# Kernel optimization log

Measured on AMD Instinct MI355X. Metric: run time of the kernel, lower is better.

The kernel has to match this reference:

```python
import jax, jax.numpy as jnp
import numpy as np

B, P, D, C = 1024, 4, 512, 128  # batch, parts, feat_dim, num_classes


def setup_inputs() -> dict:
    key = jax.random.key(0)
    k1, k2 = jax.random.split(key)
    # scale 0.05 keeps dot products O(1) so exp() stays in fp32 range
    inputs = jax.random.normal(k1, (B, P, D), dtype=jnp.float32) * 0.05
    targets = jax.random.randint(k2, (B,), 0, C, dtype=jnp.int64)
    return {"inputs": inputs, "targets": targets}


def _npairs_loss(inputs, targets):
    b, p, d = inputs.shape
    n = b * p
    X = inputs.reshape(n, d)
    t = jnp.repeat(targets, p)              # (n,) class label per row
    parts = jnp.tile(jnp.arange(p), b)      # (n,) part id per row
    prod = X @ X.T                          # (n, n) similarities

    sc = t[:, None] == t[None, :]           # same class
    sp = parts[:, None] == parts[None, :]   # same attention part
    s_sadc = (~sc) & sp
    s_dasc = sc & (~sp)
    s_dadc = (~sc) & (~sp)

    e_pos = jnp.exp(prod)                   # exp(neg) terms
    e_neg = jnp.exp(-prod)                  # exp(-pos) terms

    def group_loss(pos_mask, neg_mask):
        # sum_i sum_{j in pos_i} log(1 + sum_{k in neg_i} exp(prod[i,k] - prod[i,j]))
        # = sum log1p(S_i * exp(-prod[i,j])) with S_i = sum_{k in neg_i} exp(prod[i,k])
        S = jnp.sum(jnp.where(neg_mask, e_pos, 0.0), axis=1)        # (n,)
        terms = jnp.where(pos_mask, jnp.log1p(S[:, None] * e_neg), 0.0)
        return jnp.sum(terms)

    loss_sadc = group_loss(s_sadc, s_dadc)
    loss_dasc = group_loss(s_dasc, s_dadc)
    # NOTE: original returns loss_sadc twice and never uses loss_sasc (bug kept for fidelity)
    return (loss_sadc + loss_sadc + loss_dasc) / n


def reference(inputs, targets):
    return _npairs_loss(inputs, targets)
```

## Files before the change

### kernel.cpp

```cpp
#include <hip/hip_runtime.h>
#include <stdint.h>

#define GLOBAL_AS __attribute__((address_space(1)))
#define LDS_AS    __attribute__((address_space(3)))

typedef __attribute__((ext_vector_type(8))) __bf16 bf16x8;
typedef __attribute__((ext_vector_type(4))) float  f32x4;

static_assert(sizeof(bf16x8) == 16, "bf16x8 must be 16B");

constexpr int N  = 4096;
constexpr int DK = 512;


__global__ void k_convert(const float* __restrict__ X, __bf16* __restrict__ Xb,
                          const int* __restrict__ tbuf, int* __restrict__ cls) {
    if (blockIdx.x == 1024) {
        __shared__ int is64;
        const int t = threadIdx.x;
        if (t == 0) is64 = 1;
        __syncthreads();
        if (tbuf[4 * t + 1] != 0 || tbuf[4 * t + 3] != 0) is64 = 0;
        __syncthreads();
        const int f = is64;
#pragma unroll
        for (int q = 0; q < 4; ++q) {
            const int ti = 4 * t + q;
            const int v = tbuf[f ? 2 * ti : ti];
            cls[4 * ti + 0] = v; cls[4 * ti + 1] = v;
            cls[4 * ti + 2] = v; cls[4 * ti + 3] = v;
        }
        return;
    }
    int idx = blockIdx.x * blockDim.x + threadIdx.x;
    const float4* s = (const float4*)X;
    float4 a = s[2 * idx + 0];
    float4 b = s[2 * idx + 1];
    bf16x8 o;
    o[0] = (__bf16)a.x; o[1] = (__bf16)a.y; o[2] = (__bf16)a.z; o[3] = (__bf16)a.w;
    o[4] = (__bf16)b.x; o[5] = (__bf16)b.y; o[6] = (__bf16)b.z; o[7] = (__bf16)b.w;
    *(bf16x8*)(Xb + 8 * idx) = o;
}

__launch_bounds__(512, 4)
__global__ void k_main(const __bf16* __restrict__ Xb, const int* __restrict__ cls,
                       float* __restrict__ partials) {
    __shared__ __align__(16) __bf16 As[2][128 * 64];
    __shared__ __align__(16) __bf16 Bs[2][128 * 64];
    __shared__ float4 accR[4][128];
    __shared__ float4 accC[2][128];
    __shared__ int rowcls[128], colcls[128];

    const int tid  = threadIdx.x;
    const int lane = tid & 63;
    const int wid  = tid >> 6;
    const int wr   = wid >> 2;
    const int wc   = wid & 3;

    const int bid = blockIdx.x;
    int rt = (int)((sqrtf(8.0f * (float)bid + 1.0f) - 1.0f) * 0.5f);
    while (((rt + 1) * (rt + 2)) / 2 <= bid) ++rt;
    while ((rt * (rt + 1)) / 2 > bid) --rt;
    const int g  = bid - (rt * (rt + 1)) / 2;
    const int i0 = rt * 128;
    const int j0 = g * 128;
    const bool offdiag = (rt != g);

    if (tid < 128) {
        rowcls[tid] = cls[i0 + tid];
        colcls[tid] = cls[j0 + tid];
    }

    f32x4 acc[4][2] = {};

    const char* xb   = (const char*)Xb;
    const int   srow = tid >> 3;
    const int   skb  = ((tid & 7) ^ (srow & 7)) * 16;
    const int   ldst = wid * 1024;
    const int   rA   = lane & 15;
    const int   kgrp = lane >> 4;

#define STAGE(buf, kt)                                                                         \
    {                                                                                          \
        const size_t kb0 = (size_t)(kt) * 128;                                                 \
        char* AsB = (char*)(&As[(buf)][0]);                                                    \
        char* BsB = (char*)(&Bs[(buf)][0]);                                                    \
        _Pragma("unroll")                                                                      \
        for (int t = 0; t < 2; ++t) {                                                          \
            __builtin_amdgcn_global_load_lds(                                                  \
                (const GLOBAL_AS void*)(xb + (size_t)(i0 + t * 64 + srow) * 1024 + kb0 + skb), \
                (LDS_AS void*)(AsB + t * 8192 + ldst), 16, 0, 0);                              \
            __builtin_amdgcn_global_load_lds(                                                  \
                (const GLOBAL_AS void*)(xb + (size_t)(j0 + t * 64 + srow) * 1024 + kb0 + skb), \
                (LDS_AS void*)(BsB + t * 8192 + ldst), 16, 0, 0);                              \
        }                                                                                      \
    }

    STAGE(0, 0);
    __syncthreads();

    int cur = 0;
#pragma unroll
    for (int kt = 0; kt < DK / 64; ++kt) {
        if (kt < DK / 64 - 1) STAGE(cur ^ 1, kt + 1);
        const char* A_ = (const char*)(&As[cur][0]);
        const char* B_ = (const char*)(&Bs[cur][0]);
#pragma unroll
        for (int kk = 0; kk < 2; ++kk) {
            bf16x8 af[4];
            bf16x8 bg[2];
#pragma unroll
            for (int m = 0; m < 4; ++m) {
                const int r = wr * 64 + m * 16 + rA;
                af[m] = *(const bf16x8*)(A_ + r * 128 + (((kk * 4 + kgrp) ^ (r & 7)) * 16));
            }
#pragma unroll
            for (int n = 0; n < 2; ++n) {
                const int r = wc * 32 + n * 16 + rA;
                bg[n] = *(const bf16x8*)(B_ + r * 128 + (((kk * 4 + kgrp) ^ (r & 7)) * 16));
            }
#pragma unroll
            for (int m = 0; m < 4; ++m)
#pragma unroll
                for (int n = 0; n < 2; ++n)
                    acc[m][n] = __builtin_amdgcn_mfma_f32_16x16x32_bf16(af[m], bg[n],
                                                                        acc[m][n], 0, 0, 0);
        }
        if (kt < DK / 64 - 1) {
            __syncthreads();
            cur ^= 1;
        }
    }
#undef STAGE

    const int pj = rA & 3;
    int cj[2];
#pragma unroll
    for (int n = 0; n < 2; ++n) cj[n] = colcls[wc * 32 + n * 16 + rA];
    float cS[2] = {0.f, 0.f}, cP[2] = {0.f, 0.f}, cE[2] = {0.f, 0.f}, cW[2] = {0.f, 0.f};

#pragma unroll
    for (int m = 0; m < 4; ++m) {
        const int rbase = wr * 64 + m * 16 + kgrp * 4;
        int ci[4];
#pragma unroll
        for (int r = 0; r < 4; ++r) ci[r] = rowcls[rbase + r];
        float sS[4] = {0.f, 0.f, 0.f, 0.f};
        float sP[4] = {0.f, 0.f, 0.f, 0.f};
        float sE[4] = {0.f, 0.f, 0.f, 0.f};
        float sW[4] = {0.f, 0.f, 0.f, 0.f};
#pragma unroll
        for (int n = 0; n < 2; ++n) {
#pragma unroll
            for (int r = 0; r < 4; ++r) {
                const float p  = acc[m][n][r];
                const float ep = __expf(p);
                const bool sc = (ci[r] == cj[n]);
                const bool sp = (r == pj);
                if (!sc && !sp) { sS[r] += ep; cS[n] += ep; }
                const float w = (!sc && sp) ? 2.f : ((sc && !sp) ? 1.f : 0.f);
                sP[r] += w * p;  sE[r] += w * ep;  sW[r] += w;
                cP[n] += w * p;  cE[n] += w * ep;  cW[n] += w;
            }
        }
#pragma unroll
        for (int r = 0; r < 4; ++r) {
            float vS = sS[r], vP = sP[r], vE = sE[r], vW = sW[r];
#pragma unroll
            for (int off = 1; off < 16; off <<= 1) {
                vS += __shfl_xor(vS, off);
                vP += __shfl_xor(vP, off);
                vE += __shfl_xor(vE, off);
                vW += __shfl_xor(vW, off);
            }
            if (rA == 0) accR[wc][rbase + r] = make_float4(vS, vP, vE, vW);
        }
    }

    {
#pragma unroll
        for (int n = 0; n < 2; ++n) {
            float vS = cS[n], vP = cP[n], vE = cE[n], vW = cW[n];
            vS += __shfl_xor(vS, 16); vS += __shfl_xor(vS, 32);
            vP += __shfl_xor(vP, 16); vP += __shfl_xor(vP, 32);
            vE += __shfl_xor(vE, 16); vE += __shfl_xor(vE, 32);
            vW += __shfl_xor(vW, 16); vW += __shfl_xor(vW, 32);
            if (kgrp == 0) accC[wr][wc * 32 + n * 16 + rA] = make_float4(vS, vP, vE, vW);
        }
    }

    __syncthreads();
    if (tid < 128) {
        float4 a0 = accR[0][tid], a1 = accR[1][tid], a2 = accR[2][tid], a3 = accR[3][tid];
        float4 o = make_float4(a0.x + a1.x + a2.x + a3.x, a0.y + a1.y + a2.y + a3.y,
                               a0.z + a1.z + a2.z + a3.z, a0.w + a1.w + a2.w + a3.w);
        ((float4*)partials)[(size_t)(i0 + tid) * 32 + g] = o;
        if (offdiag) {
            float4 c0 = accC[0][tid], c1 = accC[1][tid];
            float4 oc = make_float4(c0.x + c1.x, c0.y + c1.y, c0.z + c1.z, c0.w + c1.w);
            ((float4*)partials)[(size_t)(j0 + tid) * 32 + rt] = oc;
        }
    }
}

__global__ void k_rowloss(const float* __restrict__ partials, float* __restrict__ blockSums) {
    __shared__ float red[16];
    const int tid = threadIdx.x;
    const int sub = tid & 15;
    const int row = blockIdx.x * 16 + (tid >> 4);

    const float4* p = ((const float4*)partials) + (size_t)row * 32;
    float4 a = p[sub];
    float4 b = p[sub + 16];
    float S = a.x + b.x, P = a.y + b.y, E = a.z + b.z, W = a.w + b.w;
#pragma unroll
    for (int off = 1; off < 16; off <<= 1) {
        S += __shfl_xor(S, off);
        P += __shfl_xor(P, off);
        E += __shfl_xor(E, off);
        W += __shfl_xor(W, off);
    }
    if (sub == 0) red[tid >> 4] = W * logf(S) - P + E / S;
    __syncthreads();
    if (tid == 0) {
        float s = 0.f;
#pragma unroll
        for (int r = 0; r < 16; ++r) s += red[r];
        blockSums[blockIdx.x] = s;
    }
}

__global__ void k_final2(const float* __restrict__ blockSums, float* __restrict__ out) {
    const int t = threadIdx.x;
    float v = blockSums[t] + blockSums[t + 64] + blockSums[t + 128] + blockSums[t + 192];
#pragma unroll
    for (int off = 1; off < 64; off <<= 1) v += __shfl_xor(v, off);
    if (t == 0) out[0] = v / (float)N;
}

extern "C" void kernel_launch(void* const* d_in, const int* in_sizes, int n_in,
                              void* d_out, int out_size, void* d_ws, size_t ws_size,
                              hipStream_t stream) {
    const float* X = (const float*)d_in[0];
    const int*   T = (const int*)d_in[1];
    float* out = (float*)d_out;

    char* ws = (char*)d_ws;
    __bf16* Xb     = (__bf16*)ws;
    int*    cls    = (int*)(ws + (size_t)4 * 1024 * 1024);
    float*  parts  = (float*)(ws + (size_t)4 * 1024 * 1024 + 16 * 1024);
    float*  bsums  = (float*)ws;

    hipLaunchKernelGGL(k_convert, dim3(1025), dim3(256), 0, stream, X, Xb, T, cls);
    hipLaunchKernelGGL(k_main,    dim3(528),  dim3(512), 0, stream, Xb, cls, parts);
    hipLaunchKernelGGL(k_rowloss, dim3(256),  dim3(256), 0, stream, parts, bsums);
    hipLaunchKernelGGL(k_final2,  dim3(1),    dim3(64),  0, stream, bsums, out);
}
```

Before: 59.12 us.

## Transpose MFMA output layout and remap block ids across XCDs

```diff
diff --git a/kernel.cpp b/kernel.cpp
--- a/kernel.cpp
+++ b/kernel.cpp
@@ -57,7 +57,7 @@
     const int wr   = wid >> 2;
     const int wc   = wid & 3;
 
-    const int bid = blockIdx.x;
+    const int bid = (blockIdx.x & 7) * 66 + (blockIdx.x >> 3);
     int rt = (int)((sqrtf(8.0f * (float)bid + 1.0f) - 1.0f) * 0.5f);
     while (((rt + 1) * (rt + 2)) / 2 <= bid) ++rt;
     while ((rt * (rt + 1)) / 2 > bid) --rt;
@@ -123,7 +123,7 @@
             for (int m = 0; m < 4; ++m)
 #pragma unroll
                 for (int n = 0; n < 2; ++n)
-                    acc[m][n] = __builtin_amdgcn_mfma_f32_16x16x32_bf16(af[m], bg[n],
+                    acc[m][n] = __builtin_amdgcn_mfma_f32_16x16x32_bf16(bg[n], af[m],
                                                                         acc[m][n], 0, 0, 0);
         }
         if (kt < DK / 64 - 1) {
@@ -133,60 +133,54 @@
     }
 #undef STAGE
 
-    const int pj = rA & 3;
-    int cj[2];
-#pragma unroll
-    for (int n = 0; n < 2; ++n) cj[n] = colcls[wc * 32 + n * 16 + rA];
-    float cS[2] = {0.f, 0.f}, cP[2] = {0.f, 0.f}, cE[2] = {0.f, 0.f}, cW[2] = {0.f, 0.f};
-
-#pragma unroll
-    for (int m = 0; m < 4; ++m) {
-        const int rbase = wr * 64 + m * 16 + kgrp * 4;
-        int ci[4];
-#pragma unroll
-        for (int r = 0; r < 4; ++r) ci[r] = rowcls[rbase + r];
-        float sS[4] = {0.f, 0.f, 0.f, 0.f};
-        float sP[4] = {0.f, 0.f, 0.f, 0.f};
-        float sE[4] = {0.f, 0.f, 0.f, 0.f};
-        float sW[4] = {0.f, 0.f, 0.f, 0.f};
-#pragma unroll
-        for (int n = 0; n < 2; ++n) {
-#pragma unroll
-            for (int r = 0; r < 4; ++r) {
+    const int pi = rA & 3;
+    int ci[4];
+#pragma unroll
+    for (int m = 0; m < 4; ++m) ci[m] = rowcls[wr * 64 + m * 16 + rA];
+
+    float rS[4] = {0.f, 0.f, 0.f, 0.f};
+    float rP[4] = {0.f, 0.f, 0.f, 0.f};
+    float rE[4] = {0.f, 0.f, 0.f, 0.f};
+    float rW[4] = {0.f, 0.f, 0.f, 0.f};
+
+#pragma unroll
+    for (int n = 0; n < 2; ++n) {
+#pragma unroll
+        for (int r = 0; r < 4; ++r) {
+            const int cj = colcls[wc * 32 + n * 16 + kgrp * 4 + r];
+            float cS = 0.f, cP = 0.f, cE = 0.f, cW = 0.f;
+#pragma unroll
+            for (int m = 0; m < 4; ++m) {
                 const float p  = acc[m][n][r];
                 const float ep = __expf(p);
-                const bool sc = (ci[r] == cj[n]);
-                const bool sp = (r == pj);
-                if (!sc && !sp) { sS[r] += ep; cS[n] += ep; }
+                const bool sc = (ci[m] == cj);
+                const bool sp = (pi == r);
+                if (!sc && !sp) { rS[m] += ep; cS += ep; }
                 const float w = (!sc && sp) ? 2.f : ((sc && !sp) ? 1.f : 0.f);
-                sP[r] += w * p;  sE[r] += w * ep;  sW[r] += w;
-                cP[n] += w * p;  cE[n] += w * ep;  cW[n] += w;
-            }
-        }
-#pragma unroll
-        for (int r = 0; r < 4; ++r) {
-            float vS = sS[r], vP = sP[r], vE = sE[r], vW = sW[r];
-#pragma unroll
-            for (int off = 1; off < 16; off <<= 1) {
-                vS += __shfl_xor(vS, off);
-                vP += __shfl_xor(vP, off);
-                vE += __shfl_xor(vE, off);
-                vW += __shfl_xor(vW, off);
-            }
-            if (rA == 0) accR[wc][rbase + r] = make_float4(vS, vP, vE, vW);
-        }
-    }
-
-    {
-#pragma unroll
-        for (int n = 0; n < 2; ++n) {
-            float vS = cS[n], vP = cP[n], vE = cE[n], vW = cW[n];
-            vS += __shfl_xor(vS, 16); vS += __shfl_xor(vS, 32);
-            vP += __shfl_xor(vP, 16); vP += __shfl_xor(vP, 32);
-            vE += __shfl_xor(vE, 16); vE += __shfl_xor(vE, 32);
-            vW += __shfl_xor(vW, 16); vW += __shfl_xor(vW, 32);
-            if (kgrp == 0) accC[wr][wc * 32 + n * 16 + rA] = make_float4(vS, vP, vE, vW);
-        }
+                rP[m] += w * p;  rE[m] += w * ep;  rW[m] += w;
+                cP += w * p;     cE += w * ep;     cW += w;
+            }
+            if (offdiag) {
+#pragma unroll
+                for (int off = 1; off < 16; off <<= 1) {
+                    cS += __shfl_xor(cS, off);
+                    cP += __shfl_xor(cP, off);
+                    cE += __shfl_xor(cE, off);
+                    cW += __shfl_xor(cW, off);
+                }
+                if (rA == 0)
+                    accC[wr][wc * 32 + n * 16 + kgrp * 4 + r] = make_float4(cS, cP, cE, cW);
+            }
+        }
+    }
+#pragma unroll
+    for (int m = 0; m < 4; ++m) {
+        float vS = rS[m], vP = rP[m], vE = rE[m], vW = rW[m];
+        vS += __shfl_xor(vS, 16); vS += __shfl_xor(vS, 32);
+        vP += __shfl_xor(vP, 16); vP += __shfl_xor(vP, 32);
+        vE += __shfl_xor(vE, 16); vE += __shfl_xor(vE, 32);
+        vW += __shfl_xor(vW, 16); vW += __shfl_xor(vW, 32);
+        if (kgrp == 0) accR[wc][wr * 64 + m * 16 + rA] = make_float4(vS, vP, vE, vW);
     }
 
     __syncthreads();
```

After: 47.61 us. -19.5%, faster.
